# Optimization experiments

Measured on AMD Instinct MI355X. Metric: run time of the kernel, lower is better.

## Reference

```python
import jax, jax.numpy as jnp
import numpy as np

B, NPER, F, D, E, NUM_STEPS = 256, 512, 256, 32, 524288, 4
N = B * NPER
INIT_TAU, TAU_SCALE, STEP_ALPHA = 0.1, 0.5, 5.0


def setup_inputs() -> dict:
    key = jax.random.key(0)
    ks = jax.random.split(key, 10)
    x_start = jax.random.uniform(ks[0], (N,), jnp.float32, 0.1, 1.0)   # strictly positive iterate
    x_solution = jax.random.uniform(ks[1], (N,), jnp.float32, 0.0, 1.0)
    q = jax.random.normal(ks[2], (N,), jnp.float32)
    edge_src = jax.random.randint(ks[3], (E,), 0, N, jnp.int32)
    edge_dst = jax.random.randint(ks[4], (E,), 0, N, jnp.int32)
    vals_batch = jnp.repeat(jnp.arange(B, dtype=jnp.int32), NPER)      # equal-sized graphs
    proj_matrix = jax.random.normal(ks[5], (B, NPER, F), jnp.float32) / np.float32(np.sqrt(NPER))
    W_in = jax.random.normal(ks[6], (2, D), jnp.float32) / np.float32(np.sqrt(2.0))
    b_in = jnp.zeros((D,), jnp.float32)
    W_msg = jax.random.normal(ks[7], (D, D), jnp.float32) / np.float32(np.sqrt(D))
    b_msg = jnp.zeros((D,), jnp.float32)
    W_out = jax.random.normal(ks[8], (D, 1), jnp.float32) / np.float32(np.sqrt(D))
    b_out = jnp.zeros((1,), jnp.float32)
    return {"x_start": x_start, "x_solution": x_solution, "q": q,
            "proj_matrix": proj_matrix, "W_in": W_in, "b_in": b_in,
            "W_msg": W_msg, "b_msg": b_msg, "W_out": W_out, "b_out": b_out,
            "edge_src": edge_src, "edge_dst": edge_dst, "vals_batch": vals_batch}


def _l1_normalize(x, batch):
    # per-graph L1 normalization: x / sum_i |x_i| over the graph segment
    s = jax.ops.segment_sum(jnp.abs(x), batch, num_segments=B)
    return x / (s[batch] + 1e-12)


def _line_search(x, d, batch, max_alpha):
    # largest per-graph alpha s.t. x + alpha*d >= 0, capped at max_alpha
    ratio = jnp.where(d < 0, x / jnp.maximum(-d, 1e-12), max_alpha)
    a = jnp.clip(jax.ops.segment_min(ratio, batch, num_segments=B), 0.0, max_alpha)
    return a[batch]  # gathered back to per-node


def _gnn(xs, q, edge_src, edge_dst, W_in, b_in, W_msg, b_msg, W_out, b_out):
    h = jax.nn.relu(jnp.stack([xs, q], axis=-1) @ W_in + b_in)      # [N, D]
    m = h[edge_src] @ W_msg + b_msg                                  # [E, D]
    agg = jax.ops.segment_sum(m, edge_dst, num_segments=N)          # [N, D]
    h2 = jax.nn.relu(h + agg)
    return h2 @ W_out[:, 0] + b_out[0]                               # [N]


def reference(x_start, x_solution, q, proj_matrix, W_in, b_in, W_msg, b_msg,
              W_out, b_out, edge_src, edge_dst, vals_batch):
    tau = INIT_TAU
    xs = x_start
    preds, labels = [], []
    for _ in range(NUM_STEPS):
        pred = _gnn(xs, q, edge_src, edge_dst, W_in, b_in, W_msg, b_msg, W_out, b_out)
        preds.append(pred)
        labels.append(_l1_normalize(x_solution - xs, vals_batch))
        p = _l1_normalize(jax.lax.stop_gradient(pred), vals_batch)   # .detach() in torch
        direction = p + 3.0 * tau / (xs + tau)
        tau = max(tau * TAU_SCALE, 1e-5)
        # to_dense_batch with equal graph sizes == reshape; project onto nullspace basis
        dd = direction.reshape(B, NPER)
        df = jnp.einsum('bnf,bn->bf', proj_matrix, dd)               # [B, F]
        pproj = jnp.einsum('bnf,bf->bn', proj_matrix, df).reshape(-1)  # [N]
        alpha = _line_search(xs, pproj, vals_batch, STEP_ALPHA) * 0.995
        xs = xs + alpha * pproj
    return jnp.stack(preds, axis=1), jnp.stack(labels, axis=1)       # each [N, NUM_STEPS]
```

## Files before the change

kernel.cpp:

```cpp
#include <hip/hip_runtime.h>

#define BB 256
#define NPER 512
#define FF 256
#define DD 32
#define EE 524288
#define NN (BB*NPER)
#define NSTEPS 4

__device__ __forceinline__ float bflo(unsigned u) { return __uint_as_float(u << 16); }
__device__ __forceinline__ float bfhi(unsigned u) { return __uint_as_float(u & 0xFFFF0000u); }
__device__ __forceinline__ unsigned rtn_bf16(unsigned u) {
    return (u + 0x7FFFu + ((u >> 16) & 1u)) >> 16;
}


__global__ void k_degpack(const int* __restrict__ dst, unsigned* __restrict__ deg,
                          const float* __restrict__ xs0, const float* __restrict__ q,
                          float2* __restrict__ xq) {
    int t = blockIdx.x * blockDim.x + threadIdx.x;
    if (t < NN) { float2 v; v.x = xs0[t]; v.y = q[t]; xq[t] = v; }
    atomicAdd(&deg[dst[t]], 1u);
}

__global__ __launch_bounds__(256) void k_alloc(const unsigned* __restrict__ deg,
                                               unsigned* __restrict__ gcur,
                                               unsigned* __restrict__ rowstart,
                                               unsigned* __restrict__ cursor) {
    __shared__ unsigned r[256];
    __shared__ unsigned base;
    int t = threadIdx.x;
    int i = blockIdx.x * 256 + t;
    unsigned d = deg[i];
    r[t] = d;
    __syncthreads();
    for (int o = 1; o < 256; o <<= 1) {
        unsigned v = (t >= o) ? r[t - o] : 0u;
        __syncthreads();
        r[t] += v;
        __syncthreads();
    }
    if (t == 255) base = atomicAdd(gcur, r[255]);
    __syncthreads();
    unsigned excl = r[t] - d + base;
    rowstart[i] = excl;
    cursor[i] = excl;
}

__global__ void k_fill(const int* __restrict__ src, const int* __restrict__ dst,
                       unsigned* __restrict__ cursor, int* __restrict__ csr_src) {
    int e = blockIdx.x * blockDim.x + threadIdx.x;
    unsigned pos = atomicAdd(&cursor[dst[e]], 1u);
    csr_src[pos] = src[e];
}


template<int STEP>
__global__ void k_node_g(const float2* __restrict__ xq,
                         const float* __restrict__ Win, const float* __restrict__ bin,
                         const unsigned* __restrict__ rowstart, const unsigned* __restrict__ deg,
                         const int* __restrict__ csr_src,
                         const float* __restrict__ Wmsg, const float* __restrict__ bmsg,
                         const float* __restrict__ Wout, const float* __restrict__ bout,
                         float* __restrict__ pred, float* __restrict__ out_preds) {
    int tid = threadIdx.x;
    int d = tid & 31;
    int i = blockIdx.x * 8 + (tid >> 5);
    float w0 = Win[d], w1 = Win[DD + d], b0 = bin[d];
    float wcol[DD];
    #pragma unroll
    for (int k = 0; k < DD; ++k) wcol[k] = Wmsg[k * DD + d];
    unsigned rs = rowstart[i];
    unsigned dg = deg[i];
    unsigned nfull = dg < 32u ? dg : 32u;
    float xv = 0.f, qv = 0.f;
    if ((unsigned)d < nfull) {
        int sv = csr_src[rs + d];
        float2 v = xq[sv];
        xv = v.x; qv = v.y;
    }
    float s = 0.f;
    for (unsigned j = 0; j < nfull; ++j) {
        float xj = __shfl(xv, (int)j, 32);
        float qj = __shfl(qv, (int)j, 32);
        s += fmaxf(xj * w0 + qj * w1 + b0, 0.f);
    }
    for (unsigned j = 32; j < dg; ++j) {
        int sv = csr_src[rs + j];
        float2 v = xq[sv];
        s += fmaxf(v.x * w0 + v.y * w1 + b0, 0.f);
    }
    float2 self = xq[i];
    float hval = fmaxf(self.x * w0 + self.y * w1 + b0, 0.f);
    float agg = (float)dg * bmsg[d];
    #pragma unroll
    for (int k = 0; k < DD; ++k) agg += __shfl(s, k, 32) * wcol[k];
    float h2 = fmaxf(hval + agg, 0.f);
    float v = h2 * Wout[d];
    for (int o = 16; o > 0; o >>= 1) v += __shfl_down(v, o, 32);
    if (d == 0) {
        float pr = v + bout[0];
        pred[i] = pr;
        out_preds[i * NSTEPS + STEP] = pr;
    }
}

template<int STEP0>
__global__ __launch_bounds__(1024) void k_stepF(const float* __restrict__ Pf,
                                                unsigned short* __restrict__ Pbf,
                                                float2* __restrict__ xq,
                                                const float* __restrict__ xsol,
                                                const float* __restrict__ pred,
                                                float* __restrict__ out_labels,
                                                float tau, int step, int last) {
    __shared__ float dd_l[NPER], x_l[NPER], pp_l[NPER];
    __shared__ float sl[16 * FF];
    __shared__ float dfl[FF];
    __shared__ float redA[16], redB[16];
    int b = blockIdx.x;
    int t = threadIdx.x;
    int w = t >> 6, lane = t & 63;
    int gbase = b * NPER;

    float x = 0.f, r = 0.f, p = 0.f, a1 = 0.f, a2 = 0.f;
    if (t < NPER) {
        x = xq[gbase + t].x;
        r = xsol[gbase + t] - x;
        p = pred[gbase + t];
        a1 = fabsf(r); a2 = fabsf(p);
    }
    #pragma unroll
    for (int o = 32; o > 0; o >>= 1) {
        a1 += __shfl_down(a1, o, 64);
        a2 += __shfl_down(a2, o, 64);
    }
    if (lane == 0) { redA[w] = a1; redB[w] = a2; }
    __syncthreads();
    float Sr = 1e-12f, Sp = 1e-12f;
    #pragma unroll
    for (int k = 0; k < 16; ++k) { Sr += redA[k]; Sp += redB[k]; }
    if (t < NPER) {
        out_labels[(size_t)(gbase + t) * NSTEPS + step] = r / Sr;
        x_l[t] = x;
        dd_l[t] = p / Sp + 3.0f * tau / (x + tau);
    }
    __syncthreads();

    size_t pbase = ((size_t)(gbase + w * 32)) * FF + 4 * lane;
    float4 acc = {0.f, 0.f, 0.f, 0.f};
    if (STEP0) {
        const float4* Pr = (const float4*)(Pf + pbase);
        uint2* Pw = (uint2*)(Pbf + pbase);
        #pragma unroll
        for (int nb = 0; nb < 4; ++nb) {
            float4 pv[8];
            #pragma unroll
            for (int k = 0; k < 8; ++k) pv[k] = Pr[(size_t)(nb * 8 + k) * 64];
            #pragma unroll
            for (int k = 0; k < 8; ++k) {
                int n = nb * 8 + k;
                float sc = dd_l[w * 32 + n];
                acc.x += pv[k].x * sc; acc.y += pv[k].y * sc;
                acc.z += pv[k].z * sc; acc.w += pv[k].w * sc;
                unsigned u0 = rtn_bf16(__float_as_uint(pv[k].x));
                unsigned u1 = rtn_bf16(__float_as_uint(pv[k].y));
                unsigned u2 = rtn_bf16(__float_as_uint(pv[k].z));
                unsigned u3 = rtn_bf16(__float_as_uint(pv[k].w));
                uint2 o2; o2.x = u0 | (u1 << 16); o2.y = u2 | (u3 << 16);
                Pw[(size_t)n * 64] = o2;
            }
        }
    } else {
        const uint2* Pr = (const uint2*)(Pbf + pbase);
        #pragma unroll
        for (int nb = 0; nb < 4; ++nb) {
            uint2 pv[8];
            #pragma unroll
            for (int k = 0; k < 8; ++k) pv[k] = Pr[(size_t)(nb * 8 + k) * 64];
            #pragma unroll
            for (int k = 0; k < 8; ++k) {
                float sc = dd_l[w * 32 + nb * 8 + k];
                acc.x += bflo(pv[k].x) * sc; acc.y += bfhi(pv[k].x) * sc;
                acc.z += bflo(pv[k].y) * sc; acc.w += bfhi(pv[k].y) * sc;
            }
        }
    }
    ((float4*)sl)[w * 64 + lane] = acc;
    __syncthreads();
    if (t < FF) {
        float v = 0.f;
        #pragma unroll
        for (int k = 0; k < 16; ++k) v += sl[k * FF + t];
        dfl[t] = v;
    }
    __syncthreads();

    {
        int g = t >> 5, l5 = t & 31;
        float4 dfa = ((const float4*)dfl)[l5 * 2];
        float4 dfb4 = ((const float4*)dfl)[l5 * 2 + 1];
        const uint4* Pr4 = (const uint4*)(Pbf + (size_t)(gbase + g * 16) * FF) + l5;
        #pragma unroll
        for (int nb = 0; nb < 4; ++nb) {
            uint4 pv[4];
            #pragma unroll
            for (int k = 0; k < 4; ++k) pv[k] = Pr4[(size_t)(nb * 4 + k) * 32];
            #pragma unroll
            for (int k = 0; k < 4; ++k) {
                float a = bflo(pv[k].x) * dfa.x + bfhi(pv[k].x) * dfa.y
                        + bflo(pv[k].y) * dfa.z + bfhi(pv[k].y) * dfa.w
                        + bflo(pv[k].z) * dfb4.x + bfhi(pv[k].z) * dfb4.y
                        + bflo(pv[k].w) * dfb4.z + bfhi(pv[k].w) * dfb4.w;
                #pragma unroll
                for (int o = 16; o > 0; o >>= 1) a += __shfl_down(a, o, 32);
                if (l5 == 0) pp_l[g * 16 + nb * 4 + k] = a;
            }
        }
    }
    __syncthreads();

    float d = 0.f, m = 5.0f;
    if (t < NPER) {
        d = pp_l[t];
        m = (d < 0.f) ? (x_l[t] / fmaxf(-d, 1e-12f)) : 5.0f;
    }
    #pragma unroll
    for (int o = 32; o > 0; o >>= 1) m = fminf(m, __shfl_down(m, o, 64));
    if (lane == 0) redA[w] = m;
    __syncthreads();
    float mm = redA[0];
    #pragma unroll
    for (int k = 1; k < 16; ++k) mm = fminf(mm, redA[k]);
    float alpha = fminf(fmaxf(mm, 0.f), 5.0f) * 0.995f;
    float xnew = 0.f;
    if (t < NPER) {
        xnew = x_l[t] + alpha * d;
        xq[gbase + t].x = xnew;
    }
    if (last) {
        float rr = 0.f, aa = 0.f;
        if (t < NPER) { rr = xsol[gbase + t] - xnew; aa = fabsf(rr); }
        #pragma unroll
        for (int o = 32; o > 0; o >>= 1) aa += __shfl_down(aa, o, 64);
        __syncthreads();
        if (lane == 0) redB[w] = aa;
        __syncthreads();
        float Sr2 = 1e-12f;
        #pragma unroll
        for (int k = 0; k < 16; ++k) Sr2 += redB[k];
        if (t < NPER) out_labels[(size_t)(gbase + t) * NSTEPS + (NSTEPS - 1)] = rr / Sr2;
    }
}


extern "C" void kernel_launch(void* const* d_in, const int* in_sizes, int n_in,
                              void* d_out, int out_size, void* d_ws, size_t ws_size,
                              hipStream_t stream) {
    const float* x_start = (const float*)d_in[0];
    const float* x_sol   = (const float*)d_in[1];
    const float* q       = (const float*)d_in[2];
    const float* P       = (const float*)d_in[3];
    const float* Win     = (const float*)d_in[4];
    const float* bin     = (const float*)d_in[5];
    const float* Wmsg    = (const float*)d_in[6];
    const float* bmsg    = (const float*)d_in[7];
    const float* Wout    = (const float*)d_in[8];
    const float* bout    = (const float*)d_in[9];
    const int*   esrc    = (const int*)d_in[10];
    const int*   edst    = (const int*)d_in[11];

    float* out_preds  = (float*)d_out;
    float* out_labels = (float*)d_out + (size_t)NN * NSTEPS;

    float* w = (float*)d_ws;
    unsigned* deg  = (unsigned*)w; w += NN;
    unsigned* gcur = (unsigned*)w; w += 2;
    float2* xq  = (float2*)w; w += 2 * (size_t)NN;
    float* pred  = w; w += NN;
    unsigned* rowstart = (unsigned*)w; w += NN;
    unsigned* cursor   = (unsigned*)w; w += NN;
    int* csr_src       = (int*)w;      w += EE;
    unsigned short* Pbf = (unsigned short*)w;

    hipMemsetAsync(deg, 0, (NN + 2) * sizeof(unsigned), stream);
    k_degpack<<<EE / 256, 256, 0, stream>>>(edst, deg, x_start, q, xq);
    k_alloc<<<NN / 256, 256, 0, stream>>>(deg, gcur, rowstart, cursor);
    k_fill<<<EE / 256, 256, 0, stream>>>(esrc, edst, cursor, csr_src);

    float tau = 0.1f;
    for (int step = 0; step < NSTEPS; ++step) {
        switch (step) {
        case 0: k_node_g<0><<<NN / 8, 256, 0, stream>>>(xq, Win, bin, rowstart, deg, csr_src,
                                                        Wmsg, bmsg, Wout, bout, pred, out_preds); break;
        case 1: k_node_g<1><<<NN / 8, 256, 0, stream>>>(xq, Win, bin, rowstart, deg, csr_src,
                                                        Wmsg, bmsg, Wout, bout, pred, out_preds); break;
        case 2: k_node_g<2><<<NN / 8, 256, 0, stream>>>(xq, Win, bin, rowstart, deg, csr_src,
                                                        Wmsg, bmsg, Wout, bout, pred, out_preds); break;
        default: k_node_g<3><<<NN / 8, 256, 0, stream>>>(xq, Win, bin, rowstart, deg, csr_src,
                                                         Wmsg, bmsg, Wout, bout, pred, out_preds); break;
        }
        if (step < NSTEPS - 1) {
            int last = (step == NSTEPS - 2) ? 1 : 0;
            if (step == 0)
                k_stepF<1><<<BB, 1024, 0, stream>>>(P, Pbf, xq, x_sol, pred,
                                                    out_labels, tau, step, last);
            else
                k_stepF<0><<<BB, 1024, 0, stream>>>(P, Pbf, xq, x_sol, pred,
                                                    out_labels, tau, step, last);
        }
        tau = fmaxf(tau * 0.5f, 1e-5f);
    }
}
```

Baseline: 500.5 us.

## Fuse GNN node pass into per-graph step kernel with double-buffered iterate

The per-node GNN forward pass now runs inside the per-graph projection/line-search kernel. Each 1024-thread block computes predictions for its own 512 nodes and keeps them in shared memory, so the separate node kernel and the global pred round trip go away. The iterate is double-buffered (xqA/xqB), so neighbour gathers across graphs read the previous step's values while the new ones are written. A final MODE 2 launch computes only preds and labels, replacing the old last-step label epilogue. The cost is that the gather-heavy GNN phase now runs on just 256 blocks instead of many small ones, which lowers latency hiding for the random neighbour loads and delays the start of the projection-matrix streaming.

```diff
diff --git a/kernel.cpp b/kernel.cpp
--- a/kernel.cpp
+++ b/kernel.cpp
@@ -54,65 +54,25 @@
     csr_src[pos] = src[e];
 }
 
-
-template<int STEP>
-__global__ void k_node_g(const float2* __restrict__ xq,
-                         const float* __restrict__ Win, const float* __restrict__ bin,
-                         const unsigned* __restrict__ rowstart, const unsigned* __restrict__ deg,
-                         const int* __restrict__ csr_src,
-                         const float* __restrict__ Wmsg, const float* __restrict__ bmsg,
-                         const float* __restrict__ Wout, const float* __restrict__ bout,
-                         float* __restrict__ pred, float* __restrict__ out_preds) {
-    int tid = threadIdx.x;
-    int d = tid & 31;
-    int i = blockIdx.x * 8 + (tid >> 5);
-    float w0 = Win[d], w1 = Win[DD + d], b0 = bin[d];
-    float wcol[DD];
-    #pragma unroll
-    for (int k = 0; k < DD; ++k) wcol[k] = Wmsg[k * DD + d];
-    unsigned rs = rowstart[i];
-    unsigned dg = deg[i];
-    unsigned nfull = dg < 32u ? dg : 32u;
-    float xv = 0.f, qv = 0.f;
-    if ((unsigned)d < nfull) {
-        int sv = csr_src[rs + d];
-        float2 v = xq[sv];
-        xv = v.x; qv = v.y;
-    }
-    float s = 0.f;
-    for (unsigned j = 0; j < nfull; ++j) {
-        float xj = __shfl(xv, (int)j, 32);
-        float qj = __shfl(qv, (int)j, 32);
-        s += fmaxf(xj * w0 + qj * w1 + b0, 0.f);
-    }
-    for (unsigned j = 32; j < dg; ++j) {
-        int sv = csr_src[rs + j];
-        float2 v = xq[sv];
-        s += fmaxf(v.x * w0 + v.y * w1 + b0, 0.f);
-    }
-    float2 self = xq[i];
-    float hval = fmaxf(self.x * w0 + self.y * w1 + b0, 0.f);
-    float agg = (float)dg * bmsg[d];
-    #pragma unroll
-    for (int k = 0; k < DD; ++k) agg += __shfl(s, k, 32) * wcol[k];
-    float h2 = fmaxf(hval + agg, 0.f);
-    float v = h2 * Wout[d];
-    for (int o = 16; o > 0; o >>= 1) v += __shfl_down(v, o, 32);
-    if (d == 0) {
-        float pr = v + bout[0];
-        pred[i] = pr;
-        out_preds[i * NSTEPS + STEP] = pr;
-    }
-}
-
-template<int STEP0>
-__global__ __launch_bounds__(1024) void k_stepF(const float* __restrict__ Pf,
-                                                unsigned short* __restrict__ Pbf,
-                                                float2* __restrict__ xq,
-                                                const float* __restrict__ xsol,
-                                                const float* __restrict__ pred,
-                                                float* __restrict__ out_labels,
-                                                float tau, int step, int last) {
+template<int MODE>
+__global__ __launch_bounds__(1024) void k_mega(const float* __restrict__ Pf,
+                                               unsigned short* __restrict__ Pbf,
+                                               const float2* __restrict__ xq_cur,
+                                               float2* __restrict__ xq_nxt,
+                                               const float* __restrict__ xsol,
+                                               const float* __restrict__ Win,
+                                               const float* __restrict__ bin,
+                                               const float* __restrict__ Wmsg,
+                                               const float* __restrict__ bmsg,
+                                               const float* __restrict__ Wout,
+                                               const float* __restrict__ bout,
+                                               const unsigned* __restrict__ rowstart,
+                                               const unsigned* __restrict__ deg,
+                                               const int* __restrict__ csr_src,
+                                               float* __restrict__ out_preds,
+                                               float* __restrict__ out_labels,
+                                               float tau, int step) {
+    __shared__ float pred_l[NPER];
     __shared__ float dd_l[NPER], x_l[NPER], pp_l[NPER];
     __shared__ float sl[16 * FF];
     __shared__ float dfl[FF];
@@ -122,11 +82,60 @@
     int w = t >> 6, lane = t & 63;
     int gbase = b * NPER;
 
+    {
+        int d = lane & 31;
+        int half = lane >> 5;
+        float w0 = Win[d], w1 = Win[DD + d], b0 = bin[d];
+        float wcol[DD];
+        #pragma unroll
+        for (int k = 0; k < DD; ++k) wcol[k] = Wmsg[k * DD + d];
+        float wo = Wout[d];
+        for (int pass = 0; pass < 16; ++pass) {
+            int node = pass * 32 + w * 2 + half;
+            int i = gbase + node;
+            unsigned rs = rowstart[i];
+            unsigned dg = deg[i];
+            unsigned nfull = dg < 32u ? dg : 32u;
+            float xv = 0.f, qv = 0.f;
+            if ((unsigned)d < nfull) {
+                int sv = csr_src[rs + d];
+                float2 v = xq_cur[sv];
+                xv = v.x; qv = v.y;
+            }
+            float s = 0.f;
+            for (unsigned j = 0; j < nfull; ++j) {
+                float xj = __shfl(xv, (int)j, 32);
+                float qj = __shfl(qv, (int)j, 32);
+                s += fmaxf(xj * w0 + qj * w1 + b0, 0.f);
+            }
+            for (unsigned j = 32; j < dg; ++j) {
+                int sv = csr_src[rs + j];
+                float2 v = xq_cur[sv];
+                s += fmaxf(v.x * w0 + v.y * w1 + b0, 0.f);
+            }
+            float2 self = xq_cur[i];
+            float hval = fmaxf(self.x * w0 + self.y * w1 + b0, 0.f);
+            float agg = (float)dg * bmsg[d];
+            #pragma unroll
+            for (int k = 0; k < DD; ++k) agg += __shfl(s, k, 32) * wcol[k];
+            float h2 = fmaxf(hval + agg, 0.f);
+            float v = h2 * wo;
+            #pragma unroll
+            for (int o = 16; o > 0; o >>= 1) v += __shfl_down(v, o, 32);
+            if (d == 0) {
+                float pr = v + bout[0];
+                pred_l[node] = pr;
+                out_preds[(size_t)i * NSTEPS + step] = pr;
+            }
+        }
+    }
+    __syncthreads();
+
     float x = 0.f, r = 0.f, p = 0.f, a1 = 0.f, a2 = 0.f;
     if (t < NPER) {
-        x = xq[gbase + t].x;
+        x = xq_cur[gbase + t].x;
         r = xsol[gbase + t] - x;
-        p = pred[gbase + t];
+        p = pred_l[t];
         a1 = fabsf(r); a2 = fabsf(p);
     }
     #pragma unroll
@@ -139,8 +148,9 @@
     float Sr = 1e-12f, Sp = 1e-12f;
     #pragma unroll
     for (int k = 0; k < 16; ++k) { Sr += redA[k]; Sp += redB[k]; }
+    if (t < NPER) out_labels[(size_t)(gbase + t) * NSTEPS + step] = r / Sr;
+    if (MODE == 2) return;
     if (t < NPER) {
-        out_labels[(size_t)(gbase + t) * NSTEPS + step] = r / Sr;
         x_l[t] = x;
         dd_l[t] = p / Sp + 3.0f * tau / (x + tau);
     }
@@ -148,7 +158,7 @@
 
     size_t pbase = ((size_t)(gbase + w * 32)) * FF + 4 * lane;
     float4 acc = {0.f, 0.f, 0.f, 0.f};
-    if (STEP0) {
+    if (MODE == 0) {
         const float4* Pr = (const float4*)(Pf + pbase);
         uint2* Pw = (uint2*)(Pbf + pbase);
         #pragma unroll
@@ -232,23 +242,11 @@
     #pragma unroll
     for (int k = 1; k < 16; ++k) mm = fminf(mm, redA[k]);
     float alpha = fminf(fmaxf(mm, 0.f), 5.0f) * 0.995f;
-    float xnew = 0.f;
     if (t < NPER) {
-        xnew = x_l[t] + alpha * d;
-        xq[gbase + t].x = xnew;
-    }
-    if (last) {
-        float rr = 0.f, aa = 0.f;
-        if (t < NPER) { rr = xsol[gbase + t] - xnew; aa = fabsf(rr); }
-        #pragma unroll
-        for (int o = 32; o > 0; o >>= 1) aa += __shfl_down(aa, o, 64);
-        __syncthreads();
-        if (lane == 0) redB[w] = aa;
-        __syncthreads();
-        float Sr2 = 1e-12f;
-        #pragma unroll
-        for (int k = 0; k < 16; ++k) Sr2 += redB[k];
-        if (t < NPER) out_labels[(size_t)(gbase + t) * NSTEPS + (NSTEPS - 1)] = rr / Sr2;
+        float2 o2;
+        o2.x = x_l[t] + alpha * d;
+        o2.y = xq_cur[gbase + t].y;
+        xq_nxt[gbase + t] = o2;
     }
 }
 
@@ -275,39 +273,28 @@
     float* w = (float*)d_ws;
     unsigned* deg  = (unsigned*)w; w += NN;
     unsigned* gcur = (unsigned*)w; w += 2;
-    float2* xq  = (float2*)w; w += 2 * (size_t)NN;
-    float* pred  = w; w += NN;
+    float2* xqA = (float2*)w; w += 2 * (size_t)NN;
+    float2* xqB = (float2*)w; w += 2 * (size_t)NN;
     unsigned* rowstart = (unsigned*)w; w += NN;
     unsigned* cursor   = (unsigned*)w; w += NN;
     int* csr_src       = (int*)w;      w += EE;
     unsigned short* Pbf = (unsigned short*)w;
 
     hipMemsetAsync(deg, 0, (NN + 2) * sizeof(unsigned), stream);
-    k_degpack<<<EE / 256, 256, 0, stream>>>(edst, deg, x_start, q, xq);
+    k_degpack<<<EE / 256, 256, 0, stream>>>(edst, deg, x_start, q, xqA);
     k_alloc<<<NN / 256, 256, 0, stream>>>(deg, gcur, rowstart, cursor);
     k_fill<<<EE / 256, 256, 0, stream>>>(esrc, edst, cursor, csr_src);
 
-    float tau = 0.1f;
-    for (int step = 0; step < NSTEPS; ++step) {
-        switch (step) {
-        case 0: k_node_g<0><<<NN / 8, 256, 0, stream>>>(xq, Win, bin, rowstart, deg, csr_src,
-                                                        Wmsg, bmsg, Wout, bout, pred, out_preds); break;
-        case 1: k_node_g<1><<<NN / 8, 256, 0, stream>>>(xq, Win, bin, rowstart, deg, csr_src,
-                                                        Wmsg, bmsg, Wout, bout, pred, out_preds); break;
-        case 2: k_node_g<2><<<NN / 8, 256, 0, stream>>>(xq, Win, bin, rowstart, deg, csr_src,
-                                                        Wmsg, bmsg, Wout, bout, pred, out_preds); break;
-        default: k_node_g<3><<<NN / 8, 256, 0, stream>>>(xq, Win, bin, rowstart, deg, csr_src,
-                                                         Wmsg, bmsg, Wout, bout, pred, out_preds); break;
-        }
-        if (step < NSTEPS - 1) {
-            int last = (step == NSTEPS - 2) ? 1 : 0;
-            if (step == 0)
-                k_stepF<1><<<BB, 1024, 0, stream>>>(P, Pbf, xq, x_sol, pred,
-                                                    out_labels, tau, step, last);
-            else
-                k_stepF<0><<<BB, 1024, 0, stream>>>(P, Pbf, xq, x_sol, pred,
-                                                    out_labels, tau, step, last);
-        }
-        tau = fmaxf(tau * 0.5f, 1e-5f);
-    }
-}
+    k_mega<0><<<BB, 1024, 0, stream>>>(P, Pbf, xqA, xqB, x_sol, Win, bin, Wmsg, bmsg,
+                                       Wout, bout, rowstart, deg, csr_src,
+                                       out_preds, out_labels, 0.1f, 0);
+    k_mega<1><<<BB, 1024, 0, stream>>>(P, Pbf, xqB, xqA, x_sol, Win, bin, Wmsg, bmsg,
+                                       Wout, bout, rowstart, deg, csr_src,
+                                       out_preds, out_labels, 0.05f, 1);
+    k_mega<1><<<BB, 1024, 0, stream>>>(P, Pbf, xqA, xqB, x_sol, Win, bin, Wmsg, bmsg,
+                                       Wout, bout, rowstart, deg, csr_src,
+                                       out_preds, out_labels, 0.025f, 2);
+    k_mega<2><<<BB, 1024, 0, stream>>>(P, Pbf, xqB, (float2*)nullptr, x_sol, Win, bin,
+                                       Wmsg, bmsg, Wout, bout, rowstart, deg, csr_src,
+                                       out_preds, out_labels, 0.0125f, 3);
+}
```

Result: no change. 493.9 us (-1.3%).
